# Performance work log

Hardware: AMD Instinct MI355X
Metric: run time of the kernel (lower is better)

The kernel has to match this reference:

```python
import jax, jax.numpy as jnp
import numpy as np

B, N, D, NH = 16, 512, 4096, 16
DK = D // NH  # 256; note N must equal 2*DK for the bias broadcast to be valid


def setup_inputs() -> dict:
    key = jax.random.key(0)
    ks = jax.random.split(key, 7)
    s = 1.0 / np.sqrt(D).astype(np.float32)
    return {
        "x": jax.random.normal(ks[0], (B, N, D), dtype=jnp.float32),
        "Augementation_embedding": jax.random.normal(ks[1], (B, N, D), dtype=jnp.float32),
        "Wq": jax.random.normal(ks[2], (D, D), dtype=jnp.float32) * s,
        "Wk": jax.random.normal(ks[3], (D, D), dtype=jnp.float32) * s,
        "Wv": jax.random.normal(ks[4], (D, D), dtype=jnp.float32) * s,
        "Wp": jax.random.normal(ks[5], (2 * D, D), dtype=jnp.float32) * s,
        "bp": jax.random.normal(ks[6], (2 * D,), dtype=jnp.float32) * 0.01,
    }


def reference(x, Augementation_embedding, Wq, Wk, Wv, Wp, bp):
    b, n, d = x.shape
    nh, dk = NH, DK
    scale = 1.0 / np.sqrt(dk)
    # torch nn.Linear computes x @ W.T
    q = (x @ Wq.T).reshape(b, n, nh, dk).transpose(0, 2, 1, 3)  # (b,nh,n,dk)
    k = (x @ Wk.T).reshape(b, n, nh, dk).transpose(0, 2, 1, 3)
    v = (x @ Wv.T).reshape(b, n, nh, dk).transpose(0, 2, 1, 3)
    # additive learned bias: (b,nh,n,2*dk) == (b,nh,n,n) since n == 2*dk
    ep = (Augementation_embedding @ Wp.T + bp).reshape(b, n, nh, 2 * dk).transpose(0, 2, 1, 3)
    dist = jnp.einsum("bhqd,bhkd->bhqk", q, k) * scale + ep  # (b,nh,n,n)
    dist = jax.nn.softmax(dist, axis=-1)
    att = jnp.einsum("bhqk,bhkd->bhqd", dist, v)  # (b,nh,n,dk)
    return att.transpose(0, 2, 1, 3).reshape(b, n, d)
```

## Files before the change

kernel.cpp:

```cpp
#include <hip/hip_runtime.h>
#include <hip/hip_bf16.h>

typedef __attribute__((ext_vector_type(4))) float f32x4;
typedef __attribute__((ext_vector_type(8))) short s16x8;
typedef __attribute__((ext_vector_type(4))) short s16x4;
typedef __attribute__((ext_vector_type(8))) unsigned short u16x8;
typedef __attribute__((ext_vector_type(4))) unsigned short u16x4;
typedef __attribute__((ext_vector_type(4))) float fv4;

#define DEV static __device__ __forceinline__

DEV unsigned short f2bf(float f) {
  union { float f; unsigned u; } v; v.f = f;
  return (unsigned short)((v.u + 0x7fffu + ((v.u >> 16) & 1u)) >> 16);
}
DEV float bf2f(unsigned short u) {
  union { unsigned u; float f; } v; v.u = ((unsigned)u) << 16; return v.f;
}

typedef const __attribute__((address_space(1))) void* gas_t;
typedef __attribute__((address_space(3))) void* las_t;
DEV void load_lds16(const void* g, void* l) {
  __builtin_amdgcn_global_load_lds((gas_t)g, (las_t)l, 16, 0, 0);
}

__global__ __launch_bounds__(256) void cvt_kernel(const float* __restrict__ in,
                                                  unsigned short* __restrict__ out,
                                                  int n4) {
  int i = blockIdx.x * 256 + threadIdx.x;
  int stride = gridDim.x * 256;
  for (; i < n4; i += stride) {
    fv4 v = *(const fv4*)(in + (size_t)i * 4);
    u16x4 o;
    o[0] = f2bf(v[0]); o[1] = f2bf(v[1]); o[2] = f2bf(v[2]); o[3] = f2bf(v[3]);
    *(u16x4*)(out + (size_t)i * 4) = o;
  }
}

template<int EPI>
__global__ __launch_bounds__(512, 2) void gemm256(const unsigned short* __restrict__ A,
                                                  const unsigned short* __restrict__ B,
                                                  unsigned short* __restrict__ C,
                                                  const float* __restrict__ bias,
                                                  int N, int K, int bysh, int bxpsh) {
  __shared__ unsigned short lds[4][2][8192];
  const int t = threadIdx.x;
  const int lane = t & 63;
  const int w = t >> 6;
  const int wr = w >> 1, wc = w & 1;
  const int wr2 = w >> 2;
  const int wc2 = w & 3;
  const int r0 = lane & 15;
  const int g = lane >> 4;

  const int bid = blockIdx.x;
  const int xcd = bid & 7;
  const int j = bid >> 3;
  const int by = j & ((1 << bysh) - 1);
  const int bx = (xcd << bxpsh) + (j >> bysh);
  const long brow = (long)by * 256;
  const long bcol = (long)bx * 256;

  const int srow = t >> 2;
  const int scol = ((t & 3) ^ ((t >> 3) & 3)) * 8;
  const unsigned short* As = A + (brow + srow) * (long)K + scol;
  const unsigned short* Bs = B + (bcol + srow) * (long)K + scol;
  const int d0 = t * 8;

#define STAGE(kt, bufi)                                                 \
  do {                                                                  \
    const long k0_ = (long)(kt) << 5;                                   \
    load_lds16(As + k0_,                 &lds[bufi][0][d0]);            \
    load_lds16(As + 128 * (long)K + k0_, &lds[bufi][0][d0 + 4096]);     \
    load_lds16(Bs + k0_,                 &lds[bufi][1][d0]);            \
    load_lds16(Bs + 128 * (long)K + k0_, &lds[bufi][1][d0 + 4096]);     \
  } while (0)

  f32x4 acc[8][4] = {};
  const int NT = K >> 5;

  STAGE(0, 0); STAGE(1, 1); STAGE(2, 2);
  asm volatile("s_waitcnt vmcnt(8)" ::: "memory");
  __builtin_amdgcn_s_barrier();
  __builtin_amdgcn_sched_barrier(0);

  const int cswz = (g ^ ((r0 >> 1) & 3)) * 8;
  const int arow = wr2 * 128 + r0;
  const int brw = wc2 * 64 + r0;

  for (int kt = 0; kt < NT; ++kt) {
    const unsigned short* lA = &lds[kt & 3][0][0];
    const unsigned short* lB = &lds[kt & 3][1][0];
    if (kt + 3 < NT) STAGE(kt + 3, (kt + 3) & 3);
    s16x8 av[8], bv[4];
#pragma unroll
    for (int m = 0; m < 8; ++m)
      av[m] = *(const s16x8*)&lA[(arow + m * 16) * 32 + cswz];
#pragma unroll
    for (int n = 0; n < 4; ++n)
      bv[n] = *(const s16x8*)&lB[(brw + n * 16) * 32 + cswz];
    __builtin_amdgcn_s_setprio(1);
#pragma unroll
    for (int m = 0; m < 8; ++m)
#pragma unroll
      for (int n = 0; n < 4; ++n)
        acc[m][n] = __builtin_amdgcn_mfma_f32_16x16x32_bf16(av[m], bv[n], acc[m][n], 0, 0, 0);
    __builtin_amdgcn_s_setprio(0);
    const int rem = NT - 1 - kt;
    if (rem >= 3)      asm volatile("s_waitcnt vmcnt(8)" ::: "memory");
    else if (rem == 2) asm volatile("s_waitcnt vmcnt(4)" ::: "memory");
    else if (rem == 1) asm volatile("s_waitcnt vmcnt(0)" ::: "memory");
    __builtin_amdgcn_s_barrier();
    __builtin_amdgcn_sched_barrier(0);
  }
#undef STAGE

  const int g4 = g * 4;
#pragma unroll
  for (int m = 0; m < 8; ++m) {
#pragma unroll
    for (int n = 0; n < 4; ++n) {
      f32x4 v = acc[m][n];
      long col = bcol + wc2 * 64 + n * 16 + r0;
#pragma unroll
      for (int r = 0; r < 4; ++r) {
        long row = brow + wr2 * 128 + m * 16 + g4 + r;
        float val = v[r];
        if (EPI == 1) val += bias[col];
        if (EPI == 2) {
          long addr = ((col >> 9) << 21) + (row << 9) + (col & 511);
          C[addr] = f2bf(val);
        } else {
          C[row * (long)N + col] = f2bf(val);
        }
      }
    }
  }
}

__global__ __launch_bounds__(512, 2) void attn_kernel(const unsigned short* __restrict__ Q,
                                                      const unsigned short* __restrict__ K,
                                                      const unsigned short* __restrict__ V,
                                                      const unsigned short* __restrict__ EP,
                                                      float* __restrict__ out) {
  __shared__ unsigned short lds[256 * 136];
  const int t = threadIdx.x;
  const int lane = t & 63;
  const int w = t >> 6;
  const int bid = blockIdx.x;
  const int qt = bid & 3;
  const int h = (bid >> 2) & 15;
  const int b = bid >> 6;
  const int r0 = lane & 15;
  const int g = lane >> 4;

  const int qrow = qt * 128 + w * 16;

  s16x8 qf[8];
  {
    const unsigned short* qp = Q + ((size_t)(b * 512 + qrow + r0)) * 4096 + h * 256 + g * 8;
#pragma unroll
    for (int s = 0; s < 8; ++s) qf[s] = *(const s16x8*)(qp + s * 32);
  }

  f32x4 st[32];
#pragma unroll
  for (int f = 0; f < 32; ++f) st[f] = f32x4{0.f, 0.f, 0.f, 0.f};

#pragma unroll
  for (int kc = 0; kc < 4; ++kc) {
    {
      const unsigned short* kp = K + ((size_t)(b * 512 + kc * 128)) * 4096 + h * 256;
#pragma unroll
      for (int u = 0; u < 8; ++u) {
        int fidx = u * 4096 + t * 8;
        int row = fidx >> 8, c = fidx & 255;
        u16x8 v = *(const u16x8*)(kp + (size_t)row * 4096 + c);
        *(u16x8*)&lds[row * 264 + c] = v;
      }
    }
    __syncthreads();
#pragma unroll
    for (int mf = 0; mf < 8; ++mf) {
      const unsigned short* lk = &lds[(mf * 16 + r0) * 264 + g * 8];
#pragma unroll
      for (int s = 0; s < 8; ++s) {
        s16x8 af = *(const s16x8*)(lk + s * 32);
        st[kc * 8 + mf] = __builtin_amdgcn_mfma_f32_16x16x32_bf16(af, qf[s], st[kc * 8 + mf], 0, 0, 0);
      }
    }
    __syncthreads();
  }

  {
    const unsigned short* ep = EP + ((size_t)(b * 512 + qrow + r0)) * 8192 + h * 512 + g * 4;
#pragma unroll
    for (int f = 0; f < 32; ++f) {
      u16x4 e = *(const u16x4*)(ep + f * 16);
#pragma unroll
      for (int r = 0; r < 4; ++r)
        st[f][r] = st[f][r] * 0.0625f + bf2f(e[r]);
    }
  }

  float mx = -1e30f;
#pragma unroll
  for (int f = 0; f < 32; ++f)
    mx = fmaxf(mx, fmaxf(fmaxf(st[f][0], st[f][1]), fmaxf(st[f][2], st[f][3])));
  mx = fmaxf(mx, __shfl_xor(mx, 16, 64));
  mx = fmaxf(mx, __shfl_xor(mx, 32, 64));
  float sum = 0.f;
#pragma unroll
  for (int f = 0; f < 32; ++f) {
#pragma unroll
    for (int r = 0; r < 4; ++r) {
      float e = __expf(st[f][r] - mx);
      st[f][r] = e;
      sum += e;
    }
  }
  sum += __shfl_xor(sum, 16, 64);
  sum += __shfl_xor(sum, 32, 64);
  const float rinv = 1.0f / sum;

  s16x8 pb[16];
#pragma unroll
  for (int p = 0; p < 16; ++p) {
    s16x8 v;
#pragma unroll
    for (int j = 0; j < 4; ++j) {
      v[j] = (short)f2bf(st[2 * p][j] * rinv);
      v[j + 4] = (short)f2bf(st[2 * p + 1][j] * rinv);
    }
    pb[p] = v;
  }

  f32x4 acc2[16];
#pragma unroll
  for (int d = 0; d < 16; ++d) acc2[d] = f32x4{0.f, 0.f, 0.f, 0.f};

#pragma unroll
  for (int kc = 0; kc < 4; ++kc) {
    {
      const unsigned short* vp = V + ((size_t)(b * 16 + h)) * 131072 + kc * 128;
#pragma unroll
      for (int u = 0; u < 8; ++u) {
        int fidx = u * 4096 + t * 8;
        int row = fidx >> 7, c = fidx & 127;
        u16x8 vv = *(const u16x8*)(vp + (size_t)row * 512 + c);
        *(u16x8*)&lds[row * 136 + c] = vv;
      }
    }
    __syncthreads();
#pragma unroll
    for (int d = 0; d < 16; ++d) {
      const unsigned short* lv = &lds[(d * 16 + r0) * 136 + g * 4];
#pragma unroll
      for (int p = 0; p < 4; ++p) {
        s16x4 a0 = *(const s16x4*)(lv + p * 32);
        s16x4 a1 = *(const s16x4*)(lv + p * 32 + 16);
        s16x8 av;
        av[0] = a0[0]; av[1] = a0[1]; av[2] = a0[2]; av[3] = a0[3];
        av[4] = a1[0]; av[5] = a1[1]; av[6] = a1[2]; av[7] = a1[3];
        acc2[d] = __builtin_amdgcn_mfma_f32_16x16x32_bf16(av, pb[kc * 4 + p], acc2[d], 0, 0, 0);
      }
    }
    __syncthreads();
  }

  {
    float* op = out + ((size_t)(b * 512 + qrow + r0)) * 4096 + h * 256 + g * 4;
#pragma unroll
    for (int d = 0; d < 16; ++d)
      *(fv4*)(op + d * 16) = acc2[d];
  }
}

extern "C" void kernel_launch(void* const* d_in, const int* in_sizes, int n_in,
                              void* d_out, int out_size, void* d_ws, size_t ws_size,
                              hipStream_t stream) {
  const float* x   = (const float*)d_in[0];
  const float* aug = (const float*)d_in[1];
  const float* wq  = (const float*)d_in[2];
  const float* wk  = (const float*)d_in[3];
  const float* wv  = (const float*)d_in[4];
  const float* wp  = (const float*)d_in[5];
  const float* bp  = (const float*)d_in[6];
  float* out = (float*)d_out;

  const size_t OFF_XA = 0;
  const size_t OFF_WQ = 67108864;
  const size_t OFF_WK = OFF_WQ + 33554432;
  const size_t OFF_WV = OFF_WK + 33554432;
  const size_t OFF_Q  = OFF_WQ + 100663296;
  const size_t OFF_K  = OFF_Q + 67108864;
  const size_t OFF_VT = OFF_K + 67108864;
  const size_t OFF_EP = OFF_VT + 67108864;
  const size_t NEED   = OFF_EP + 134217728;
  if (ws_size < NEED) return;

  char* ws = (char*)d_ws;
  unsigned short* x_bf   = (unsigned short*)(ws + OFF_XA);
  unsigned short* aug_bf = (unsigned short*)(ws + OFF_XA);
  unsigned short* wq_bf  = (unsigned short*)(ws + OFF_WQ);
  unsigned short* wk_bf  = (unsigned short*)(ws + OFF_WK);
  unsigned short* wv_bf  = (unsigned short*)(ws + OFF_WV);
  unsigned short* wp_bf  = (unsigned short*)(ws + OFF_WQ);
  unsigned short* q_bf   = (unsigned short*)(ws + OFF_Q);
  unsigned short* k_bf   = (unsigned short*)(ws + OFF_K);
  unsigned short* vt_bf  = (unsigned short*)(ws + OFF_VT);
  unsigned short* ep_bf  = (unsigned short*)(ws + OFF_EP);

  cvt_kernel<<<2048, 256, 0, stream>>>(x, x_bf, 33554432 / 4);
  cvt_kernel<<<2048, 256, 0, stream>>>(wq, wq_bf, 16777216 / 4);
  cvt_kernel<<<2048, 256, 0, stream>>>(wk, wk_bf, 16777216 / 4);
  cvt_kernel<<<2048, 256, 0, stream>>>(wv, wv_bf, 16777216 / 4);

  gemm256<0><<<512, 512, 0, stream>>>(x_bf, wq_bf, q_bf, nullptr, 4096, 4096, 5, 1);
  gemm256<0><<<512, 512, 0, stream>>>(x_bf, wk_bf, k_bf, nullptr, 4096, 4096, 5, 1);
  gemm256<2><<<512, 512, 0, stream>>>(wv_bf, x_bf, vt_bf, nullptr, 8192, 4096, 4, 2);

  cvt_kernel<<<2048, 256, 0, stream>>>(aug, aug_bf, 33554432 / 4);
  cvt_kernel<<<2048, 256, 0, stream>>>(wp, wp_bf, 33554432 / 4);
  gemm256<1><<<1024, 512, 0, stream>>>(aug_bf, wp_bf, ep_bf, bp, 8192, 4096, 5, 2);

  attn_kernel<<<1024, 512, 0, stream>>>(q_bf, k_bf, vt_bf, ep_bf, out);
}
```

Before: 1.721 ms.

## Switch projection GEMMs to 32x32x16 MFMA and regroup block tiles per XCD

```diff
diff --git a/kernel.cpp b/kernel.cpp
--- a/kernel.cpp
+++ b/kernel.cpp
@@ -2,6 +2,7 @@
 #include <hip/hip_bf16.h>
 
 typedef __attribute__((ext_vector_type(4))) float f32x4;
+typedef __attribute__((ext_vector_type(16))) float f32x16;
 typedef __attribute__((ext_vector_type(8))) short s16x8;
 typedef __attribute__((ext_vector_type(4))) short s16x4;
 typedef __attribute__((ext_vector_type(8))) unsigned short u16x8;
@@ -42,22 +43,23 @@
                                                   const unsigned short* __restrict__ B,
                                                   unsigned short* __restrict__ C,
                                                   const float* __restrict__ bias,
-                                                  int N, int K, int bysh, int bxpsh) {
+                                                  int N, int K, int xgsh, int rbxsh) {
   __shared__ unsigned short lds[4][2][8192];
   const int t = threadIdx.x;
   const int lane = t & 63;
   const int w = t >> 6;
-  const int wr = w >> 1, wc = w & 1;
   const int wr2 = w >> 2;
   const int wc2 = w & 3;
-  const int r0 = lane & 15;
-  const int g = lane >> 4;
+  const int l31 = lane & 31;
+  const int g2 = lane >> 5;
 
   const int bid = blockIdx.x;
   const int xcd = bid & 7;
-  const int j = bid >> 3;
-  const int by = j & ((1 << bysh) - 1);
-  const int bx = (xcd << bxpsh) + (j >> bysh);
+  const int i = bid >> 3;
+  const int r = i >> 5;
+  const int s = i & 31;
+  const int by = ((xcd >> xgsh) << 3) + (s & 7);
+  const int bx = ((xcd & ((1 << xgsh) - 1)) << rbxsh) + r * 4 + (s >> 3);
   const long brow = (long)by * 256;
   const long bcol = (long)bx * 256;
 
@@ -76,7 +78,7 @@
     load_lds16(Bs + 128 * (long)K + k0_, &lds[bufi][1][d0 + 4096]);     \
   } while (0)
 
-  f32x4 acc[8][4] = {};
+  f32x16 acc[4][2] = {};
   const int NT = K >> 5;
 
   STAGE(0, 0); STAGE(1, 1); STAGE(2, 2);
@@ -84,27 +86,36 @@
   __builtin_amdgcn_s_barrier();
   __builtin_amdgcn_sched_barrier(0);
 
-  const int cswz = (g ^ ((r0 >> 1) & 3)) * 8;
-  const int arow = wr2 * 128 + r0;
-  const int brw = wc2 * 64 + r0;
+  const int sw = (l31 >> 1) & 3;
+  const int cs0 = ((0 + g2) ^ sw) * 8;
+  const int cs1 = ((2 + g2) ^ sw) * 8;
+  const int abase = (wr2 * 128 + l31) * 32;
+  const int bbase = (wc2 * 64 + l31) * 32;
 
   for (int kt = 0; kt < NT; ++kt) {
     const unsigned short* lA = &lds[kt & 3][0][0];
     const unsigned short* lB = &lds[kt & 3][1][0];
     if (kt + 3 < NT) STAGE(kt + 3, (kt + 3) & 3);
-    s16x8 av[8], bv[4];
-#pragma unroll
-    for (int m = 0; m < 8; ++m)
-      av[m] = *(const s16x8*)&lA[(arow + m * 16) * 32 + cswz];
-#pragma unroll
-    for (int n = 0; n < 4; ++n)
-      bv[n] = *(const s16x8*)&lB[(brw + n * 16) * 32 + cswz];
+    s16x8 av0[4], av1[4], bv0[2], bv1[2];
+#pragma unroll
+    for (int m = 0; m < 4; ++m) {
+      av0[m] = *(const s16x8*)&lA[abase + m * 1024 + cs0];
+      av1[m] = *(const s16x8*)&lA[abase + m * 1024 + cs1];
+    }
+#pragma unroll
+    for (int n = 0; n < 2; ++n) {
+      bv0[n] = *(const s16x8*)&lB[bbase + n * 1024 + cs0];
+      bv1[n] = *(const s16x8*)&lB[bbase + n * 1024 + cs1];
+    }
     __builtin_amdgcn_s_setprio(1);
 #pragma unroll
-    for (int m = 0; m < 8; ++m)
-#pragma unroll
-      for (int n = 0; n < 4; ++n)
-        acc[m][n] = __builtin_amdgcn_mfma_f32_16x16x32_bf16(av[m], bv[n], acc[m][n], 0, 0, 0);
+    for (int m = 0; m < 4; ++m) {
+#pragma unroll
+      for (int n = 0; n < 2; ++n) {
+        acc[m][n] = __builtin_amdgcn_mfma_f32_32x32x16_bf16(av0[m], bv0[n], acc[m][n], 0, 0, 0);
+        acc[m][n] = __builtin_amdgcn_mfma_f32_32x32x16_bf16(av1[m], bv1[n], acc[m][n], 0, 0, 0);
+      }
+    }
     __builtin_amdgcn_s_setprio(0);
     const int rem = NT - 1 - kt;
     if (rem >= 3)      asm volatile("s_waitcnt vmcnt(8)" ::: "memory");
@@ -115,18 +126,18 @@
   }
 #undef STAGE
 
-  const int g4 = g * 4;
-#pragma unroll
-  for (int m = 0; m < 8; ++m) {
-#pragma unroll
-    for (int n = 0; n < 4; ++n) {
-      f32x4 v = acc[m][n];
-      long col = bcol + wc2 * 64 + n * 16 + r0;
-#pragma unroll
-      for (int r = 0; r < 4; ++r) {
-        long row = brow + wr2 * 128 + m * 16 + g4 + r;
-        float val = v[r];
-        if (EPI == 1) val += bias[col];
+#pragma unroll
+  for (int m = 0; m < 4; ++m) {
+#pragma unroll
+    for (int n = 0; n < 2; ++n) {
+      f32x16 v = acc[m][n];
+      long col = bcol + wc2 * 64 + n * 32 + l31;
+      float bc = (EPI == 1) ? bias[col] : 0.f;
+#pragma unroll
+      for (int reg = 0; reg < 16; ++reg) {
+        long row = brow + wr2 * 128 + m * 32 + (reg & 3) + 8 * (reg >> 2) + 4 * g2;
+        float val = v[reg];
+        if (EPI == 1) val += bc;
         if (EPI == 2) {
           long addr = ((col >> 9) << 21) + (row << 9) + (col & 511);
           C[addr] = f2bf(val);
@@ -316,13 +327,13 @@
   cvt_kernel<<<2048, 256, 0, stream>>>(wk, wk_bf, 16777216 / 4);
   cvt_kernel<<<2048, 256, 0, stream>>>(wv, wv_bf, 16777216 / 4);
 
-  gemm256<0><<<512, 512, 0, stream>>>(x_bf, wq_bf, q_bf, nullptr, 4096, 4096, 5, 1);
-  gemm256<0><<<512, 512, 0, stream>>>(x_bf, wk_bf, k_bf, nullptr, 4096, 4096, 5, 1);
-  gemm256<2><<<512, 512, 0, stream>>>(wv_bf, x_bf, vt_bf, nullptr, 8192, 4096, 4, 2);
+  gemm256<0><<<512, 512, 0, stream>>>(x_bf, wq_bf, q_bf, nullptr, 4096, 4096, 1, 3);
+  gemm256<0><<<512, 512, 0, stream>>>(x_bf, wk_bf, k_bf, nullptr, 4096, 4096, 1, 3);
+  gemm256<2><<<512, 512, 0, stream>>>(wv_bf, x_bf, vt_bf, nullptr, 8192, 4096, 2, 3);
 
   cvt_kernel<<<2048, 256, 0, stream>>>(aug, aug_bf, 33554432 / 4);
   cvt_kernel<<<2048, 256, 0, stream>>>(wp, wp_bf, 33554432 / 4);
-  gemm256<1><<<1024, 512, 0, stream>>>(aug_bf, wp_bf, ep_bf, bp, 8192, 4096, 5, 2);
+  gemm256<1><<<1024, 512, 0, stream>>>(aug_bf, wp_bf, ep_bf, bp, 8192, 4096, 1, 4);
 
   attn_kernel<<<1024, 512, 0, stream>>>(q_bf, k_bf, vt_bf, ep_bf, out);
 }
```

After: 1.764 ms. 1.02x slower.
